# Performance work log

Hardware: AMD Instinct MI355X
Metric: run time of the kernel (lower is better)

## Reference

```python
import jax, jax.numpy as jnp
import numpy as np

NUM_NETS = 2_000_000
PINS_PER_NET = 4
NUM_PINS = NUM_NETS * PINS_PER_NET


def setup_inputs() -> dict:
    key = jax.random.key(0)
    k1, k2, k3 = jax.random.split(key, 3)
    num_slrX, num_slrY = 1, 4
    # pin positions already expressed in SLR-grid units: x in [0, num_slrX), y in [0, num_slrY)
    pos = jax.random.uniform(k1, (NUM_PINS, 2), jnp.float32) * jnp.array(
        [float(max(num_slrX, 1)), float(max(num_slrY, 1))], jnp.float32)
    # CSR netpin structure: each net owns PINS_PER_NET pins, flat list is a permutation of all pins
    flat_netpin = jax.random.permutation(k2, NUM_PINS).astype(jnp.int32)
    netpin_start = (jnp.arange(NUM_NETS + 1, dtype=jnp.int32) * PINS_PER_NET)
    net_ids = jnp.repeat(jnp.arange(NUM_NETS, dtype=jnp.int32), PINS_PER_NET)
    net_weights = jax.random.uniform(k3, (NUM_NETS,), jnp.float32, minval=0.5, maxval=1.5)
    net_mask = jnp.ones((NUM_NETS,), jnp.bool_)
    pin_mask = jnp.zeros((NUM_PINS,), jnp.bool_)
    inv_gamma = jnp.float32(2.0)  # 1 / gamma, gamma = 0.5
    return dict(pos=pos, flat_netpin=flat_netpin, netpin_start=netpin_start,
                net_ids=net_ids, net_weights=net_weights, net_mask=net_mask,
                pin_mask=pin_mask, inv_gamma=inv_gamma,
                num_slrX=num_slrX, num_slrY=num_slrY)


def reference(pos, flat_netpin, netpin_start, net_ids, net_weights, net_mask,
              pin_mask, inv_gamma, num_slrX, num_slrY):
    """Weighted-average SLL: per-net log-sum-exp weighted-average span of pin
    SLR coordinates, per dimension, counted only for dims with >1 SLR."""
    n = net_weights.shape[0]
    p = pos[flat_netpin]  # [P, 2] gather pin coords in CSR order
    # numerically-stable exp weights per net (segment max/min shift)
    mx = jax.ops.segment_max(p, net_ids, num_segments=n)  # [N, 2]
    mn = jax.ops.segment_min(p, net_ids, num_segments=n)  # [N, 2]
    ep = jnp.exp((p - mx[net_ids]) * inv_gamma)   # exp(+x/gamma), shifted
    en = jnp.exp((mn[net_ids] - p) * inv_gamma)   # exp(-x/gamma), shifted
    s_ep = jax.ops.segment_sum(ep, net_ids, num_segments=n)
    s_xep = jax.ops.segment_sum(p * ep, net_ids, num_segments=n)
    s_en = jax.ops.segment_sum(en, net_ids, num_segments=n)
    s_xen = jax.ops.segment_sum(p * en, net_ids, num_segments=n)
    wa = s_xep / s_ep - s_xen / s_en  # [N, 2] weighted-average span per dim
    dim_on = jnp.array([num_slrX > 1, num_slrY > 1], dtype=wa.dtype)  # only multi-SLR dims
    per_net = jnp.sum(wa * dim_on, axis=1)  # [N]
    return jnp.sum(jnp.where(net_mask, net_weights * per_net, jnp.float32(0.0)))
```

## Files before the change

### kernel.cpp

```cpp
#include <hip/hip_runtime.h>
#include <stdint.h>


#define PINB_SHIFT 15
#define PINB_SIZE  (1 << PINB_SHIFT)
#define JB_SHIFT   14
#define JB_SIZE    (1 << JB_SHIFT)
#define P1_CHUNK   4096
#define P2_CHUNK   4096
#define MAX_PINB   256
#define MAX_JB     512

__device__ __forceinline__ float wa4(float a, float b, float c, float d, float ig) {
    float ea = __expf(a * ig), eb = __expf(b * ig);
    float ec = __expf(c * ig), ed = __expf(d * ig);
    float na = __expf(-a * ig), nb = __expf(-b * ig);
    float nc = __expf(-c * ig), nd = __expf(-d * ig);
    float s_ep  = ea + eb + ec + ed;
    float s_xep = a * ea + b * eb + c * ec + d * ed;
    float s_en  = na + nb + nc + nd;
    float s_xen = a * na + b * nb + c * nc + d * nd;
    return s_xep / s_ep - s_xen / s_en;
}

__global__ void zero_out_kernel(float* __restrict__ out) { out[0] = 0.0f; }

__global__ void init_cursors_kernel(unsigned* __restrict__ cur1, int n_pinb,
                                    unsigned* __restrict__ cur2, int n_jb) {
    int t = threadIdx.x;
    for (int i = t; i < n_pinb; i += blockDim.x) cur1[i] = (unsigned)i * PINB_SIZE;
    for (int i = t; i < n_jb;   i += blockDim.x) cur2[i] = (unsigned)i * JB_SIZE;
}

__global__ __launch_bounds__(256) void p1_partition(
    const int* __restrict__ fnp, int NP, int n_pinb,
    uint2* __restrict__ ent1, unsigned* __restrict__ cur1)
{
    __shared__ uint2 staged[P1_CHUNK];
    __shared__ unsigned hist[MAX_PINB], scn[MAX_PINB];
    __shared__ unsigned lcnt[MAX_PINB], gbase[MAX_PINB];
    const int base  = blockIdx.x * P1_CHUNK;
    const int valid = min(P1_CHUNK, NP - base);
    const int t = threadIdx.x;

    if (t < n_pinb) { hist[t] = 0; lcnt[t] = 0; }
    __syncthreads();

    unsigned pins[16];
    #pragma unroll
    for (int m = 0; m < 16; ++m) {
        int k = t + 256 * m;
        pins[m] = 0u;
        if (k < valid) {
            pins[m] = (unsigned)fnp[base + k];
            atomicAdd(&hist[pins[m] >> PINB_SHIFT], 1u);
        }
    }
    __syncthreads();

    if (t < n_pinb) scn[t] = hist[t];
    __syncthreads();
    #pragma unroll
    for (int off = 1; off < MAX_PINB; off <<= 1) {
        unsigned v = 0;
        if (t < n_pinb && t >= off) v = scn[t - off];
        __syncthreads();
        if (t < n_pinb) scn[t] += v;
        __syncthreads();
    }
    if (t < n_pinb) {
        unsigned ex = scn[t] - hist[t];
        scn[t] = ex;
        gbase[t] = atomicAdd(&cur1[t], hist[t]);
    }
    __syncthreads();

    #pragma unroll
    for (int m = 0; m < 16; ++m) {
        int k = t + 256 * m;
        if (k < valid) {
            unsigned pin = pins[m];
            unsigned b = pin >> PINB_SHIFT;
            unsigned pos = scn[b] + atomicAdd(&lcnt[b], 1u);
            staged[pos] = make_uint2(pin, (unsigned)(base + k));
        }
    }
    __syncthreads();

    for (int k = t; k < valid; k += 256) {
        uint2 e = staged[k];
        unsigned b = e.x >> PINB_SHIFT;
        unsigned dst = gbase[b] + ((unsigned)k - scn[b]);
        ent1[dst] = e;
    }
}

__global__ __launch_bounds__(512) void p2_gather(
    const uint2* __restrict__ ent1, const float* __restrict__ posf,
    const int* __restrict__ slrx_p,
    int NP, int n_pinb, int n_jb,
    uint2* __restrict__ ent2, float* __restrict__ xout,
    unsigned* __restrict__ cur2)
{
    const int x   = blockIdx.x & 7;
    const int g   = blockIdx.x >> 3;
    const int r   = g >> 3;
    const int sub = g & 7;
    const int b   = x + 8 * r;
    if (b >= n_pinb) return;
    const int count_b = min(PINB_SIZE, NP - b * PINB_SIZE);
    const int sbase   = sub * P2_CHUNK;
    const int valid   = min(P2_CHUNK, count_b - sbase);
    if (valid <= 0) return;

    const bool dimx = (slrx_p[0] > 1);
    __shared__ uint2 staged[P2_CHUNK];
    __shared__ float xstag[P2_CHUNK];
    __shared__ unsigned hist[MAX_JB], scn[MAX_JB];
    __shared__ unsigned lcnt[MAX_JB], gbase[MAX_JB];
    const int t = threadIdx.x;

    if (t < n_jb) { hist[t] = 0; lcnt[t] = 0; }
    __syncthreads();

    uint2 e[8]; float yv[8], xv[8];
    const int ebase = b * PINB_SIZE + sbase;
    #pragma unroll
    for (int m = 0; m < 8; ++m) {
        int k = t + 512 * m;
        e[m] = (k < valid) ? ent1[ebase + k] : make_uint2(0u, 0u);
    }
    #pragma unroll
    for (int m = 0; m < 8; ++m) {
        int k = t + 512 * m;
        yv[m] = 0.f; xv[m] = 0.f;
        if (k < valid) {
            yv[m] = posf[2u * e[m].x + 1u];
            if (dimx) xv[m] = posf[2u * e[m].x];
        }
    }
    #pragma unroll
    for (int m = 0; m < 8; ++m) {
        int k = t + 512 * m;
        if (k < valid) atomicAdd(&hist[e[m].y >> JB_SHIFT], 1u);
    }
    __syncthreads();

    if (t < n_jb) scn[t] = hist[t];
    __syncthreads();
    #pragma unroll
    for (int off = 1; off < MAX_JB; off <<= 1) {
        unsigned v = 0;
        if (t < n_jb && t >= off) v = scn[t - off];
        __syncthreads();
        if (t < n_jb) scn[t] += v;
        __syncthreads();
    }
    if (t < n_jb) {
        unsigned ex = scn[t] - hist[t];
        scn[t] = ex;
        gbase[t] = atomicAdd(&cur2[t], hist[t]);
    }
    __syncthreads();

    #pragma unroll
    for (int m = 0; m < 8; ++m) {
        int k = t + 512 * m;
        if (k < valid) {
            unsigned jb = e[m].y >> JB_SHIFT;
            unsigned pos = scn[jb] + atomicAdd(&lcnt[jb], 1u);
            staged[pos] = make_uint2(e[m].y, __float_as_uint(yv[m]));
            if (dimx) xstag[pos] = xv[m];
        }
    }
    __syncthreads();

    for (int k = t; k < valid; k += 512) {
        uint2 s = staged[k];
        unsigned jb = s.x >> JB_SHIFT;
        unsigned dst = gbase[jb] + ((unsigned)k - scn[jb]);
        ent2[dst] = s;
        if (dimx) xout[dst] = xstag[k];
    }
}

__global__ __launch_bounds__(256) void p3_compute(
    const uint2* __restrict__ ent2, const float* __restrict__ xin,
    const float* __restrict__ wts, const float* __restrict__ ig_p,
    const int* __restrict__ slrx_p, const int* __restrict__ slry_p,
    int NP, float* __restrict__ out)
{
    __shared__ float ytmp[JB_SIZE];
    const int jb = blockIdx.x;
    const int base_j = jb * JB_SIZE;
    const int nslots = min(JB_SIZE, NP - base_j);
    const int t = threadIdx.x;
    const float ig = ig_p[0];
    const bool dimx = (slrx_p[0] > 1), dimy = (slry_p[0] > 1);
    float val = 0.f;

    if (!dimx) {
        for (int k = t; k < nslots; k += 256) {
            uint2 e = ent2[base_j + k];
            ytmp[e.x - (unsigned)base_j] = __uint_as_float(e.y);
        }
        __syncthreads();
        const int nnets = nslots >> 2, bnet = base_j >> 2;
        for (int i = t; i < nnets; i += 256) {
            float wy = wa4(ytmp[4*i], ytmp[4*i+1], ytmp[4*i+2], ytmp[4*i+3], ig);
            val += wts[bnet + i] * (dimy ? wy : 0.f);
        }
    } else {
        for (int h = 0; h < 2; ++h) {
            const int h0 = base_j + h * (JB_SIZE / 2);
            const int hn = min(JB_SIZE / 2, NP - h0);
            if (hn <= 0) break;
            __syncthreads();
            for (int k = t; k < nslots; k += 256) {
                uint2 e = ent2[base_j + k];
                int rel = (int)e.x - h0;
                if (rel >= 0 && rel < hn) {
                    ytmp[rel] = __uint_as_float(e.y);
                    ytmp[(JB_SIZE / 2) + rel] = xin[base_j + k];
                }
            }
            __syncthreads();
            const int nnets = hn >> 2, bnet = h0 >> 2;
            for (int i = t; i < nnets; i += 256) {
                float wy = wa4(ytmp[4*i], ytmp[4*i+1], ytmp[4*i+2], ytmp[4*i+3], ig);
                float wx = wa4(ytmp[(JB_SIZE/2)+4*i], ytmp[(JB_SIZE/2)+4*i+1],
                               ytmp[(JB_SIZE/2)+4*i+2], ytmp[(JB_SIZE/2)+4*i+3], ig);
                val += wts[bnet + i] * ((dimx ? wx : 0.f) + (dimy ? wy : 0.f));
            }
        }
    }

    #pragma unroll
    for (int off = 32; off > 0; off >>= 1) val += __shfl_down(val, off, 64);
    __syncthreads();
    if ((t & 63) == 0) ytmp[t >> 6] = val;
    __syncthreads();
    if (t == 0) atomicAdd(out, ytmp[0] + ytmp[1] + ytmp[2] + ytmp[3]);
}

__global__ __launch_bounds__(256) void wasll_fallback(
    const float2* __restrict__ pos, const int4* __restrict__ fnp4,
    const float* __restrict__ net_weights, const float* __restrict__ inv_gamma_p,
    const int* __restrict__ slrx_p, const int* __restrict__ slry_p,
    float* __restrict__ out, int num_nets)
{
    const float ig = inv_gamma_p[0];
    const float dx = (slrx_p[0] > 1) ? 1.0f : 0.0f;
    const float dy = (slry_p[0] > 1) ? 1.0f : 0.0f;
    int net = blockIdx.x * blockDim.x + threadIdx.x;
    float val = 0.0f;
    if (net < num_nets) {
        int4 idx = fnp4[net];
        float2 p0 = pos[idx.x], p1 = pos[idx.y], p2 = pos[idx.z], p3 = pos[idx.w];
        val = net_weights[net] * (dx * wa4(p0.x, p1.x, p2.x, p3.x, ig)
                                + dy * wa4(p0.y, p1.y, p2.y, p3.y, ig));
    }
    #pragma unroll
    for (int off = 32; off > 0; off >>= 1) val += __shfl_down(val, off, 64);
    __shared__ float smem[4];
    if ((threadIdx.x & 63) == 0) smem[threadIdx.x >> 6] = val;
    __syncthreads();
    if (threadIdx.x == 0)
        atomicAdd(out, smem[0] + smem[1] + smem[2] + smem[3]);
}

extern "C" void kernel_launch(void* const* d_in, const int* in_sizes, int n_in,
                              void* d_out, int out_size, void* d_ws, size_t ws_size,
                              hipStream_t stream) {
    const float* posf        = (const float*)d_in[0];
    const int*   fnp         = (const int*)d_in[1];
    const float* net_weights = (const float*)d_in[4];
    const float* inv_gamma   = (const float*)d_in[7];
    const int*   slrx        = (const int*)d_in[8];
    const int*   slry        = (const int*)d_in[9];
    float*       out         = (float*)d_out;
    const int    N  = in_sizes[4];
    const int    NP = in_sizes[1];

    hipLaunchKernelGGL(zero_out_kernel, dim3(1), dim3(1), 0, stream, out);

    const int n_pinb = (NP + PINB_SIZE - 1) >> PINB_SHIFT;
    const int n_jb   = (NP + JB_SIZE - 1) >> JB_SHIFT;

    size_t off = 0;
    auto carve = [&](size_t bytes) { size_t o = off; off += (bytes + 255) & ~size_t(255); return o; };
    size_t o_ent1 = carve((size_t)n_pinb * PINB_SIZE * sizeof(uint2));
    size_t o_ent2 = carve((size_t)n_jb * JB_SIZE * sizeof(uint2));
    size_t o_xout = carve((size_t)n_jb * JB_SIZE * sizeof(float));
    size_t o_cur1 = carve((size_t)n_pinb * sizeof(unsigned));
    size_t o_cur2 = carve((size_t)n_jb * sizeof(unsigned));

    const bool ok = (NP == 4 * N) && (n_pinb <= MAX_PINB) && (n_jb <= MAX_JB) &&
                    (off <= ws_size);
    if (!ok) {
        const int block = 256, grid = (N + block - 1) / block;
        hipLaunchKernelGGL(wasll_fallback, dim3(grid), dim3(block), 0, stream,
                           (const float2*)posf, (const int4*)fnp, net_weights,
                           inv_gamma, slrx, slry, out, N);
        return;
    }

    char* ws = (char*)d_ws;
    uint2*    ent1 = (uint2*)(ws + o_ent1);
    uint2*    ent2 = (uint2*)(ws + o_ent2);
    float*    xout = (float*)(ws + o_xout);
    unsigned* cur1 = (unsigned*)(ws + o_cur1);
    unsigned* cur2 = (unsigned*)(ws + o_cur2);

    hipLaunchKernelGGL(init_cursors_kernel, dim3(1), dim3(512), 0, stream,
                       cur1, n_pinb, cur2, n_jb);

    const int g1 = (NP + P1_CHUNK - 1) / P1_CHUNK;
    hipLaunchKernelGGL(p1_partition, dim3(g1), dim3(256), 0, stream,
                       fnp, NP, n_pinb, ent1, cur1);

    const int rounds = (n_pinb + 7) / 8;
    const int g2 = 8 * 8 * rounds;
    hipLaunchKernelGGL(p2_gather, dim3(g2), dim3(512), 0, stream,
                       ent1, posf, slrx, NP, n_pinb, n_jb, ent2, xout, cur2);

    hipLaunchKernelGGL(p3_compute, dim3(n_jb), dim3(256), 0, stream,
                       ent2, xout, net_weights, inv_gamma, slrx, slry, NP, out);
}
```

Measured before the change: 318.8 us.

## Stage pin-block positions in LDS and process each dimension in separate passes

The pin-bucket size drops to 8K. Each p2 block now reads its whole pin block's positions contiguously into shared memory and gathers from there, instead of doing random global reads. Partitioning uses int4 loads, one-pass atomic ranking and a wavefront-shuffle scan in place of the barrier-heavy scan. Each dimension runs its own p2/p3 pass, which skips a disabled dimension and drops the x-side buffer. The costs are more launches and a 32KB LDS window per block that may limit occupancy.

```diff
diff --git a/kernel.cpp b/kernel.cpp
--- a/kernel.cpp
+++ b/kernel.cpp
@@ -2,14 +2,14 @@
 #include <stdint.h>
 
 
-#define PINB_SHIFT 15
+#define PINB_SHIFT 13
 #define PINB_SIZE  (1 << PINB_SHIFT)
+#define MAX_PINB   1024
 #define JB_SHIFT   14
 #define JB_SIZE    (1 << JB_SHIFT)
-#define P1_CHUNK   4096
+#define MAX_JB     512
+#define P1_CHUNK   8192
 #define P2_CHUNK   4096
-#define MAX_PINB   256
-#define MAX_JB     512
 
 __device__ __forceinline__ float wa4(float a, float b, float c, float d, float ig) {
     float ea = __expf(a * ig), eb = __expf(b * ig);
@@ -23,216 +23,208 @@
     return s_xep / s_ep - s_xen / s_en;
 }
 
-__global__ void zero_out_kernel(float* __restrict__ out) { out[0] = 0.0f; }
-
-__global__ void init_cursors_kernel(unsigned* __restrict__ cur1, int n_pinb,
-                                    unsigned* __restrict__ cur2, int n_jb) {
+__global__ void init_kernel(unsigned* __restrict__ cur1, int n_pinb,
+                            unsigned* __restrict__ cur2, int n_jb,
+                            float* __restrict__ out) {
     int t = threadIdx.x;
-    for (int i = t; i < n_pinb; i += blockDim.x) cur1[i] = (unsigned)i * PINB_SIZE;
-    for (int i = t; i < n_jb;   i += blockDim.x) cur2[i] = (unsigned)i * JB_SIZE;
-}
-
-__global__ __launch_bounds__(256) void p1_partition(
-    const int* __restrict__ fnp, int NP, int n_pinb,
+    if (t == 0) out[0] = 0.0f;
+    for (int i = t; i < n_pinb; i += blockDim.x) cur1[i] = (unsigned)i << PINB_SHIFT;
+    for (int i = t; i < n_jb;   i += blockDim.x) cur2[i] = (unsigned)i << JB_SHIFT;
+}
+
+__global__ void reinit_cur2_kernel(unsigned* __restrict__ cur2, int n_jb) {
+    int t = threadIdx.x;
+    for (int i = t; i < n_jb; i += blockDim.x) cur2[i] = (unsigned)i << JB_SHIFT;
+}
+
+__global__ __launch_bounds__(512) void p1_partition(
+    const int4* __restrict__ fnp4, int NP, int n_pinb,
     uint2* __restrict__ ent1, unsigned* __restrict__ cur1)
 {
-    __shared__ uint2 staged[P1_CHUNK];
-    __shared__ unsigned hist[MAX_PINB], scn[MAX_PINB];
-    __shared__ unsigned lcnt[MAX_PINB], gbase[MAX_PINB];
+    __shared__ uint2    staged[P1_CHUNK];
+    __shared__ unsigned hist[MAX_PINB];
+    __shared__ unsigned scn[MAX_PINB];
+    __shared__ unsigned gbase[MAX_PINB];
     const int base  = blockIdx.x * P1_CHUNK;
     const int valid = min(P1_CHUNK, NP - base);
     const int t = threadIdx.x;
 
-    if (t < n_pinb) { hist[t] = 0; lcnt[t] = 0; }
-    __syncthreads();
-
-    unsigned pins[16];
-    #pragma unroll
-    for (int m = 0; m < 16; ++m) {
-        int k = t + 256 * m;
-        pins[m] = 0u;
-        if (k < valid) {
-            pins[m] = (unsigned)fnp[base + k];
-            atomicAdd(&hist[pins[m] >> PINB_SHIFT], 1u);
-        }
-    }
-    __syncthreads();
-
-    if (t < n_pinb) scn[t] = hist[t];
-    __syncthreads();
-    #pragma unroll
-    for (int off = 1; off < MAX_PINB; off <<= 1) {
-        unsigned v = 0;
-        if (t < n_pinb && t >= off) v = scn[t - off];
-        __syncthreads();
-        if (t < n_pinb) scn[t] += v;
-        __syncthreads();
-    }
-    if (t < n_pinb) {
-        unsigned ex = scn[t] - hist[t];
-        scn[t] = ex;
-        gbase[t] = atomicAdd(&cur1[t], hist[t]);
-    }
-    __syncthreads();
-
-    #pragma unroll
-    for (int m = 0; m < 16; ++m) {
-        int k = t + 256 * m;
-        if (k < valid) {
-            unsigned pin = pins[m];
-            unsigned b = pin >> PINB_SHIFT;
-            unsigned pos = scn[b] + atomicAdd(&lcnt[b], 1u);
-            staged[pos] = make_uint2(pin, (unsigned)(base + k));
-        }
-    }
-    __syncthreads();
-
-    for (int k = t; k < valid; k += 256) {
+    for (int b = t; b < MAX_PINB; b += 512) hist[b] = 0;
+    __syncthreads();
+
+    unsigned pin[16], rnk[16];
+    #pragma unroll
+    for (int m4 = 0; m4 < 4; ++m4) {
+        int k4 = t + 512 * m4;
+        int kk = 4 * k4;
+        int4 v = make_int4(0, 0, 0, 0);
+        if (kk < valid) v = fnp4[(base >> 2) + k4];
+        pin[4*m4+0] = (unsigned)v.x; pin[4*m4+1] = (unsigned)v.y;
+        pin[4*m4+2] = (unsigned)v.z; pin[4*m4+3] = (unsigned)v.w;
+    }
+    #pragma unroll
+    for (int m4 = 0; m4 < 4; ++m4)
+        #pragma unroll
+        for (int c = 0; c < 4; ++c) {
+            int kk = 4 * (t + 512 * m4) + c;
+            rnk[4*m4+c] = 0;
+            if (kk < valid)
+                rnk[4*m4+c] = atomicAdd(&hist[pin[4*m4+c] >> PINB_SHIFT], 1u);
+        }
+    __syncthreads();
+
+    if (t < 64) {
+        unsigned v[16], s = 0;
+        #pragma unroll
+        for (int i = 0; i < 16; ++i) { v[i] = hist[t * 16 + i]; s += v[i]; }
+        unsigned e = s;
+        #pragma unroll
+        for (int off = 1; off < 64; off <<= 1) {
+            unsigned u = __shfl_up(e, off, 64);
+            if (t >= off) e += u;
+        }
+        e -= s;
+        #pragma unroll
+        for (int i = 0; i < 16; ++i) { scn[t * 16 + i] = e; e += v[i]; }
+    }
+    __syncthreads();
+    for (int b = t; b < n_pinb; b += 512)
+        if (hist[b]) gbase[b] = atomicAdd(&cur1[b], hist[b]);
+    __syncthreads();
+
+    #pragma unroll
+    for (int m4 = 0; m4 < 4; ++m4)
+        #pragma unroll
+        for (int c = 0; c < 4; ++c) {
+            int kk = 4 * (t + 512 * m4) + c;
+            if (kk < valid) {
+                unsigned p = pin[4*m4+c];
+                staged[scn[p >> PINB_SHIFT] + rnk[4*m4+c]] =
+                    make_uint2(p, (unsigned)(base + kk));
+            }
+        }
+    __syncthreads();
+
+    for (int k = t; k < valid; k += 512) {
         uint2 e = staged[k];
         unsigned b = e.x >> PINB_SHIFT;
-        unsigned dst = gbase[b] + ((unsigned)k - scn[b]);
-        ent1[dst] = e;
+        ent1[gbase[b] + ((unsigned)k - scn[b])] = e;
     }
 }
 
 __global__ __launch_bounds__(512) void p2_gather(
-    const uint2* __restrict__ ent1, const float* __restrict__ posf,
-    const int* __restrict__ slrx_p,
-    int NP, int n_pinb, int n_jb,
-    uint2* __restrict__ ent2, float* __restrict__ xout,
-    unsigned* __restrict__ cur2)
+    const uint2* __restrict__ ent1, const float2* __restrict__ pos2,
+    const int* __restrict__ slrx_p, const int* __restrict__ slry_p,
+    int d, int NP, int n_jb,
+    uint2* __restrict__ ent2, unsigned* __restrict__ cur2)
 {
-    const int x   = blockIdx.x & 7;
-    const int g   = blockIdx.x >> 3;
-    const int r   = g >> 3;
-    const int sub = g & 7;
-    const int b   = x + 8 * r;
-    if (b >= n_pinb) return;
-    const int count_b = min(PINB_SIZE, NP - b * PINB_SIZE);
-    const int sbase   = sub * P2_CHUNK;
-    const int valid   = min(P2_CHUNK, count_b - sbase);
-    if (valid <= 0) return;
-
-    const bool dimx = (slrx_p[0] > 1);
-    __shared__ uint2 staged[P2_CHUNK];
-    __shared__ float xstag[P2_CHUNK];
-    __shared__ unsigned hist[MAX_JB], scn[MAX_JB];
-    __shared__ unsigned lcnt[MAX_JB], gbase[MAX_JB];
+    const int slr = (d == 0) ? slrx_p[0] : slry_p[0];
+    if (slr <= 1) return;
+
+    __shared__ float    win[PINB_SIZE];
+    __shared__ uint2    staged[P2_CHUNK];
+    __shared__ unsigned hist[MAX_JB], scn[MAX_JB], gbase[MAX_JB];
+    const int b       = blockIdx.x;
+    const int pbase   = b << PINB_SHIFT;
+    const int count_b = min(PINB_SIZE, NP - pbase);
     const int t = threadIdx.x;
 
-    if (t < n_jb) { hist[t] = 0; lcnt[t] = 0; }
-    __syncthreads();
-
-    uint2 e[8]; float yv[8], xv[8];
-    const int ebase = b * PINB_SIZE + sbase;
-    #pragma unroll
-    for (int m = 0; m < 8; ++m) {
-        int k = t + 512 * m;
-        e[m] = (k < valid) ? ent1[ebase + k] : make_uint2(0u, 0u);
-    }
-    #pragma unroll
-    for (int m = 0; m < 8; ++m) {
-        int k = t + 512 * m;
-        yv[m] = 0.f; xv[m] = 0.f;
-        if (k < valid) {
-            yv[m] = posf[2u * e[m].x + 1u];
-            if (dimx) xv[m] = posf[2u * e[m].x];
-        }
-    }
-    #pragma unroll
-    for (int m = 0; m < 8; ++m) {
-        int k = t + 512 * m;
-        if (k < valid) atomicAdd(&hist[e[m].y >> JB_SHIFT], 1u);
-    }
-    __syncthreads();
-
-    if (t < n_jb) scn[t] = hist[t];
-    __syncthreads();
-    #pragma unroll
-    for (int off = 1; off < MAX_JB; off <<= 1) {
-        unsigned v = 0;
-        if (t < n_jb && t >= off) v = scn[t - off];
-        __syncthreads();
-        if (t < n_jb) scn[t] += v;
-        __syncthreads();
-    }
-    if (t < n_jb) {
-        unsigned ex = scn[t] - hist[t];
-        scn[t] = ex;
-        gbase[t] = atomicAdd(&cur2[t], hist[t]);
-    }
-    __syncthreads();
-
-    #pragma unroll
-    for (int m = 0; m < 8; ++m) {
-        int k = t + 512 * m;
-        if (k < valid) {
-            unsigned jb = e[m].y >> JB_SHIFT;
-            unsigned pos = scn[jb] + atomicAdd(&lcnt[jb], 1u);
-            staged[pos] = make_uint2(e[m].y, __float_as_uint(yv[m]));
-            if (dimx) xstag[pos] = xv[m];
-        }
-    }
-    __syncthreads();
-
-    for (int k = t; k < valid; k += 512) {
-        uint2 s = staged[k];
-        unsigned jb = s.x >> JB_SHIFT;
-        unsigned dst = gbase[jb] + ((unsigned)k - scn[jb]);
-        ent2[dst] = s;
-        if (dimx) xout[dst] = xstag[k];
-    }
-}
-
-__global__ __launch_bounds__(256) void p3_compute(
-    const uint2* __restrict__ ent2, const float* __restrict__ xin,
-    const float* __restrict__ wts, const float* __restrict__ ig_p,
+    for (int i = t; i < count_b; i += 512) {
+        float2 p = pos2[pbase + i];
+        win[i] = d ? p.y : p.x;
+    }
+
+    #pragma unroll
+    for (int r = 0; r < PINB_SIZE / P2_CHUNK; ++r) {
+        const int cbase = r * P2_CHUNK;
+        const int valid = min(P2_CHUNK, count_b - cbase);
+        __syncthreads();
+        for (int q = t; q < MAX_JB; q += 512) hist[q] = 0;
+        __syncthreads();
+
+        uint2 e[8]; unsigned rnk[8]; float yv[8];
+        #pragma unroll
+        for (int m = 0; m < 8; ++m) {
+            int k = t + 512 * m;
+            e[m] = make_uint2(0u, 0u);
+            if (k < valid) e[m] = ent1[pbase + cbase + k];
+        }
+        #pragma unroll
+        for (int m = 0; m < 8; ++m) {
+            int k = t + 512 * m;
+            yv[m] = (k < valid) ? win[e[m].x - (unsigned)pbase] : 0.0f;
+        }
+        #pragma unroll
+        for (int m = 0; m < 8; ++m) {
+            int k = t + 512 * m;
+            rnk[m] = 0;
+            if (k < valid) rnk[m] = atomicAdd(&hist[e[m].y >> JB_SHIFT], 1u);
+        }
+        __syncthreads();
+
+        if (t < 64) {
+            unsigned v[8], s = 0;
+            #pragma unroll
+            for (int i = 0; i < 8; ++i) { v[i] = hist[t * 8 + i]; s += v[i]; }
+            unsigned ex = s;
+            #pragma unroll
+            for (int off = 1; off < 64; off <<= 1) {
+                unsigned u = __shfl_up(ex, off, 64);
+                if (t >= off) ex += u;
+            }
+            ex -= s;
+            #pragma unroll
+            for (int i = 0; i < 8; ++i) { scn[t * 8 + i] = ex; ex += v[i]; }
+        }
+        __syncthreads();
+        if (t < n_jb && hist[t]) gbase[t] = atomicAdd(&cur2[t], hist[t]);
+        __syncthreads();
+
+        #pragma unroll
+        for (int m = 0; m < 8; ++m) {
+            int k = t + 512 * m;
+            if (k < valid)
+                staged[scn[e[m].y >> JB_SHIFT] + rnk[m]] =
+                    make_uint2(e[m].y, __float_as_uint(yv[m]));
+        }
+        __syncthreads();
+
+        for (int k = t; k < valid; k += 512) {
+            uint2 s2 = staged[k];
+            unsigned jb = s2.x >> JB_SHIFT;
+            ent2[gbase[jb] + ((unsigned)k - scn[jb])] = s2;
+        }
+    }
+}
+
+__global__ __launch_bounds__(512) void p3_compute(
+    const uint2* __restrict__ ent2, const float* __restrict__ wts,
+    const float* __restrict__ ig_p,
     const int* __restrict__ slrx_p, const int* __restrict__ slry_p,
-    int NP, float* __restrict__ out)
+    int d, int NP, float* __restrict__ out)
 {
+    const int slr = (d == 0) ? slrx_p[0] : slry_p[0];
+    if (slr <= 1) return;
+
     __shared__ float ytmp[JB_SIZE];
-    const int jb = blockIdx.x;
-    const int base_j = jb * JB_SIZE;
+    const int jb     = blockIdx.x;
+    const int base_j = jb << JB_SHIFT;
     const int nslots = min(JB_SIZE, NP - base_j);
     const int t = threadIdx.x;
     const float ig = ig_p[0];
-    const bool dimx = (slrx_p[0] > 1), dimy = (slry_p[0] > 1);
-    float val = 0.f;
-
-    if (!dimx) {
-        for (int k = t; k < nslots; k += 256) {
-            uint2 e = ent2[base_j + k];
-            ytmp[e.x - (unsigned)base_j] = __uint_as_float(e.y);
-        }
-        __syncthreads();
-        const int nnets = nslots >> 2, bnet = base_j >> 2;
-        for (int i = t; i < nnets; i += 256) {
-            float wy = wa4(ytmp[4*i], ytmp[4*i+1], ytmp[4*i+2], ytmp[4*i+3], ig);
-            val += wts[bnet + i] * (dimy ? wy : 0.f);
-        }
-    } else {
-        for (int h = 0; h < 2; ++h) {
-            const int h0 = base_j + h * (JB_SIZE / 2);
-            const int hn = min(JB_SIZE / 2, NP - h0);
-            if (hn <= 0) break;
-            __syncthreads();
-            for (int k = t; k < nslots; k += 256) {
-                uint2 e = ent2[base_j + k];
-                int rel = (int)e.x - h0;
-                if (rel >= 0 && rel < hn) {
-                    ytmp[rel] = __uint_as_float(e.y);
-                    ytmp[(JB_SIZE / 2) + rel] = xin[base_j + k];
-                }
-            }
-            __syncthreads();
-            const int nnets = hn >> 2, bnet = h0 >> 2;
-            for (int i = t; i < nnets; i += 256) {
-                float wy = wa4(ytmp[4*i], ytmp[4*i+1], ytmp[4*i+2], ytmp[4*i+3], ig);
-                float wx = wa4(ytmp[(JB_SIZE/2)+4*i], ytmp[(JB_SIZE/2)+4*i+1],
-                               ytmp[(JB_SIZE/2)+4*i+2], ytmp[(JB_SIZE/2)+4*i+3], ig);
-                val += wts[bnet + i] * ((dimx ? wx : 0.f) + (dimy ? wy : 0.f));
-            }
-        }
+
+    for (int k = t; k < nslots; k += 512) {
+        uint2 e = ent2[base_j + k];
+        ytmp[e.x & (JB_SIZE - 1)] = __uint_as_float(e.y);
+    }
+    __syncthreads();
+
+    float val = 0.0f;
+    const int nnets = nslots >> 2, bnet = base_j >> 2;
+    const float4* y4 = (const float4*)ytmp;
+    for (int i = t; i < nnets; i += 512) {
+        float4 p = y4[i];
+        val += wts[bnet + i] * wa4(p.x, p.y, p.z, p.w, ig);
     }
 
     #pragma unroll
@@ -240,7 +232,12 @@
     __syncthreads();
     if ((t & 63) == 0) ytmp[t >> 6] = val;
     __syncthreads();
-    if (t == 0) atomicAdd(out, ytmp[0] + ytmp[1] + ytmp[2] + ytmp[3]);
+    if (t == 0) {
+        float s = 0.0f;
+        #pragma unroll
+        for (int w = 0; w < 8; ++w) s += ytmp[w];
+        atomicAdd(out, s);
+    }
 }
 
 __global__ __launch_bounds__(256) void wasll_fallback(
@@ -269,6 +266,8 @@
         atomicAdd(out, smem[0] + smem[1] + smem[2] + smem[3]);
 }
 
+__global__ void zero_out_kernel(float* __restrict__ out) { out[0] = 0.0f; }
+
 extern "C" void kernel_launch(void* const* d_in, const int* in_sizes, int n_in,
                               void* d_out, int out_size, void* d_ws, size_t ws_size,
                               hipStream_t stream) {
@@ -282,8 +281,6 @@
     const int    N  = in_sizes[4];
     const int    NP = in_sizes[1];
 
-    hipLaunchKernelGGL(zero_out_kernel, dim3(1), dim3(1), 0, stream, out);
-
     const int n_pinb = (NP + PINB_SIZE - 1) >> PINB_SHIFT;
     const int n_jb   = (NP + JB_SIZE - 1) >> JB_SHIFT;
 
@@ -291,13 +288,13 @@
     auto carve = [&](size_t bytes) { size_t o = off; off += (bytes + 255) & ~size_t(255); return o; };
     size_t o_ent1 = carve((size_t)n_pinb * PINB_SIZE * sizeof(uint2));
     size_t o_ent2 = carve((size_t)n_jb * JB_SIZE * sizeof(uint2));
-    size_t o_xout = carve((size_t)n_jb * JB_SIZE * sizeof(float));
     size_t o_cur1 = carve((size_t)n_pinb * sizeof(unsigned));
     size_t o_cur2 = carve((size_t)n_jb * sizeof(unsigned));
 
-    const bool ok = (NP == 4 * N) && (n_pinb <= MAX_PINB) && (n_jb <= MAX_JB) &&
-                    (off <= ws_size);
+    const bool ok = (NP == 4 * N) && (NP % 4 == 0) &&
+                    (n_pinb <= MAX_PINB) && (n_jb <= MAX_JB) && (off <= ws_size);
     if (!ok) {
+        hipLaunchKernelGGL(zero_out_kernel, dim3(1), dim3(1), 0, stream, out);
         const int block = 256, grid = (N + block - 1) / block;
         hipLaunchKernelGGL(wasll_fallback, dim3(grid), dim3(block), 0, stream,
                            (const float2*)posf, (const int4*)fnp, net_weights,
@@ -308,22 +305,25 @@
     char* ws = (char*)d_ws;
     uint2*    ent1 = (uint2*)(ws + o_ent1);
     uint2*    ent2 = (uint2*)(ws + o_ent2);
-    float*    xout = (float*)(ws + o_xout);
     unsigned* cur1 = (unsigned*)(ws + o_cur1);
     unsigned* cur2 = (unsigned*)(ws + o_cur2);
 
-    hipLaunchKernelGGL(init_cursors_kernel, dim3(1), dim3(512), 0, stream,
-                       cur1, n_pinb, cur2, n_jb);
+    hipLaunchKernelGGL(init_kernel, dim3(1), dim3(1024), 0, stream,
+                       cur1, n_pinb, cur2, n_jb, out);
 
     const int g1 = (NP + P1_CHUNK - 1) / P1_CHUNK;
-    hipLaunchKernelGGL(p1_partition, dim3(g1), dim3(256), 0, stream,
-                       fnp, NP, n_pinb, ent1, cur1);
-
-    const int rounds = (n_pinb + 7) / 8;
-    const int g2 = 8 * 8 * rounds;
-    hipLaunchKernelGGL(p2_gather, dim3(g2), dim3(512), 0, stream,
-                       ent1, posf, slrx, NP, n_pinb, n_jb, ent2, xout, cur2);
-
-    hipLaunchKernelGGL(p3_compute, dim3(n_jb), dim3(256), 0, stream,
-                       ent2, xout, net_weights, inv_gamma, slrx, slry, NP, out);
-}
+    hipLaunchKernelGGL(p1_partition, dim3(g1), dim3(512), 0, stream,
+                       (const int4*)fnp, NP, n_pinb, ent1, cur1);
+
+    hipLaunchKernelGGL(p2_gather, dim3(n_pinb), dim3(512), 0, stream,
+                       ent1, (const float2*)posf, slrx, slry, 0, NP, n_jb, ent2, cur2);
+    hipLaunchKernelGGL(p3_compute, dim3(n_jb), dim3(512), 0, stream,
+                       ent2, net_weights, inv_gamma, slrx, slry, 0, NP, out);
+
+    hipLaunchKernelGGL(reinit_cur2_kernel, dim3(1), dim3(1024), 0, stream, cur2, n_jb);
+
+    hipLaunchKernelGGL(p2_gather, dim3(n_pinb), dim3(512), 0, stream,
+                       ent1, (const float2*)posf, slrx, slry, 1, NP, n_jb, ent2, cur2);
+    hipLaunchKernelGGL(p3_compute, dim3(n_jb), dim3(512), 0, stream,
+                       ent2, net_weights, inv_gamma, slrx, slry, 1, NP, out);
+}
```

Result: faster. 278.3 us (-12.7%).
